# Optimization experiments

Measured on AMD Instinct MI355X. Metric: run time of the kernel, lower is better.

The kernel has to match this reference:

```python
import jax, jax.numpy as jnp
import numpy as np


def fps(xyz, npoint):
    # farthest point sampling, starts at index 0 (matches pointnet2 CUDA kernel)
    B, N, _ = xyz.shape
    def step(carry, _):
        min_d, last = carry
        last_xyz = jnp.take_along_axis(xyz, last[:, None, None], axis=1)  # [B,1,3]
        d = jnp.sum((xyz - last_xyz) ** 2, axis=-1)                        # [B,N]
        min_d = jnp.minimum(min_d, d)
        nxt = jnp.argmax(min_d, axis=1).astype(jnp.int32)
        return (min_d, nxt), last
    init = (jnp.full((B, N), 1e10, xyz.dtype), jnp.zeros((B,), jnp.int32))
    _, idx = jax.lax.scan(step, init, None, length=npoint)
    return jnp.transpose(idx)  # [B, npoint]


def ball_query(xyz, new_xyz, radius, nsample):
    # first nsample points within radius; pad with first hit (0 if none) -- CUDA semantics
    N = xyz.shape[1]
    d2 = jnp.sum((new_xyz[:, :, None, :] - xyz[:, None, :, :]) ** 2, axis=-1)  # [B,S,N]
    cand = jnp.where(d2 < radius * radius, jnp.arange(N, dtype=jnp.int32)[None, None, :], N)
    srt = jnp.sort(cand, axis=-1)[..., :nsample]
    first = srt[..., :1]
    first = jnp.where(first == N, 0, first)
    return jnp.where(srt == N, first, srt)  # [B,S,K]


def gather_nbrs(x, idx):
    # x [B,N,C], idx [B,S,K] -> [B,S,K,C]
    B, S, K = idx.shape
    flat = jnp.take_along_axis(x, idx.reshape(B, S * K, 1), axis=1)
    return flat.reshape(B, S, K, x.shape[-1])


def shared_mlp(x, layers):
    # 1x1 conv (+ folded eval-mode BN) + ReLU per layer
    for w, b in layers:
        x = jax.nn.relu(jnp.einsum('bskc,oc->bsko', x, w) + b)
    return x


def sa_module(xyz, feat, npoint, radius, nsample, layers):
    idx = fps(xyz, npoint)
    new_xyz = jnp.take_along_axis(xyz, idx[:, :, None], axis=1)  # [B,S,3]
    gidx = ball_query(xyz, new_xyz, radius, nsample)
    grouped = gather_nbrs(xyz, gidx) - new_xyz[:, :, None, :]    # centered local xyz
    if feat is not None:
        grouped = jnp.concatenate([grouped, gather_nbrs(feat, gidx)], axis=-1)
    x = shared_mlp(grouped, layers)
    return new_xyz, jnp.max(x, axis=2)  # max-pool over neighbors -> [B,S,Cout]


def sa_module_all(xyz, feat, layers):
    # GroupAll: concat raw (uncentered) xyz with features, one group of all points
    x = jnp.concatenate([xyz, feat], axis=-1)[:, None]  # [B,1,N,3+C]
    x = shared_mlp(x, layers)
    return jnp.max(x, axis=2)[:, 0]  # [B,Cout]


def _forward(data, ws):
    B, T, N, _ = data.shape
    xyz = data.reshape(B * T, N, 3)
    xyz, feat = sa_module(xyz, None, 256, 0.2, 32, ws[0])
    xyz, feat = sa_module(xyz, feat, 128, 0.4, 32, ws[1])
    out = sa_module_all(xyz, feat, ws[2])
    return out.reshape(B, T, -1)


DIMS = [(3, 64), (64, 64), (64, 128), (131, 128), (128, 128), (128, 256), (259, 256), (256, 512), (512, 1024)]
NAMES = ['1_0', '1_1', '1_2', '2_0', '2_1', '2_2', '3_0', '3_1', '3_2']


def setup_inputs() -> dict:
    key = jax.random.key(0)
    keys = jax.random.split(key, 1 + 2 * len(DIMS))
    inp = {'data': jax.random.normal(keys[0], (4, 8, 4096, 3), jnp.float32)}
    for i, ((cin, cout), nm) in enumerate(zip(DIMS, NAMES)):
        inp['w' + nm] = jax.random.normal(keys[1 + 2 * i], (cout, cin), jnp.float32) / np.sqrt(cin).astype(np.float32)
        inp['b' + nm] = jax.random.normal(keys[2 + 2 * i], (cout,), jnp.float32) * 0.02
    return inp


def reference(data, w1_0, b1_0, w1_1, b1_1, w1_2, b1_2,
              w2_0, b2_0, w2_1, b2_1, w2_2, b2_2,
              w3_0, b3_0, w3_1, b3_1, w3_2, b3_2):
    ws = [[(w1_0, b1_0), (w1_1, b1_1), (w1_2, b1_2)],
          [(w2_0, b2_0), (w2_1, b2_1), (w2_2, b2_2)],
          [(w3_0, b3_0), (w3_1, b3_1), (w3_2, b3_2)]]
    return _forward(data, ws)
```

## Files before the change

### kernel.cpp

```cpp
#include <hip/hip_runtime.h>
#include <hip/hip_bf16.h>
#include <cstdint>
#include <cstddef>

#define BT 32
#define N1 4096
#define S1 256
#define S2 128
#define KNB 32

typedef __attribute__((ext_vector_type(8))) short short8;
typedef __attribute__((ext_vector_type(4))) float f32x4;

__device__ __forceinline__ float sqdist(float ax, float ay, float az,
                                        float bx, float by, float bz) {
    float dx = __fsub_rn(ax, bx), dy = __fsub_rn(ay, by), dz = __fsub_rn(az, bz);
    return __fadd_rn(__fadd_rn(__fmul_rn(dx, dx), __fmul_rn(dy, dy)), __fmul_rn(dz, dz));
}

__device__ __forceinline__ unsigned short f2bf(float f) {
    unsigned u = __float_as_uint(f);
    return (unsigned short)((u + 0x7FFFu + ((u >> 16) & 1u)) >> 16);
}
__device__ __forceinline__ float bf2f(unsigned short h) {
    return __uint_as_float(((unsigned)h) << 16);
}

__device__ __forceinline__ unsigned long long packvi(float v, int idx) {
    return ((unsigned long long)__float_as_uint(v) << 32) | (unsigned)(~idx);
}

template <int CTRL>
__device__ __forceinline__ unsigned long long dppmax(unsigned long long v) {
    int lo = (int)(unsigned)(v & 0xFFFFFFFFull);
    int hi = (int)(unsigned)(v >> 32);
    int lo2 = __builtin_amdgcn_update_dpp(0, lo, CTRL, 0xF, 0xF, false);
    int hi2 = __builtin_amdgcn_update_dpp(0, hi, CTRL, 0xF, 0xF, false);
    unsigned long long o = ((unsigned long long)(unsigned)hi2 << 32) | (unsigned)lo2;
    return o > v ? o : v;
}
#define ROR1 0x121
#define ROR2 0x122
#define ROR4 0x124
#define ROR8 0x128

__global__ __launch_bounds__(256) void fps1_kernel(const float* __restrict__ xyz,
                                                   float* __restrict__ nxz) {
    const int b = blockIdx.x, tid = threadIdx.x;
    const int lane = tid & 63, wv = tid >> 6;
    const float* X = xyz + (size_t)b * (N1 * 3);
    __shared__ float4 s4[N1];
    __shared__ unsigned long long slots[2][16];
    __shared__ float hist[S1 * 3];
    float px[16], py[16], pz[16], md[16];
    int bidx[16];
#pragma unroll
    for (int j = 0; j < 16; ++j) {
        int i = tid + 256 * j;
        float x = X[i * 3 + 0], y = X[i * 3 + 1], z = X[i * 3 + 2];
        s4[i] = make_float4(x, y, z, 0.f);
        px[j] = x; py[j] = y; pz[j] = z;
        md[j] = 1e10f;
        bidx[j] = i;
    }
    if (tid == 0) { hist[0] = X[0]; hist[1] = X[1]; hist[2] = X[2]; }
    __syncthreads();
    float4 c0 = s4[0];
    float lx = c0.x, ly = c0.y, lz = c0.z;
    for (int t = 1; t < S1; ++t) {
        float bv = -1.0f; int bi = 0;
#pragma unroll
        for (int j = 0; j < 16; ++j) {
            float d = sqdist(px[j], py[j], pz[j], lx, ly, lz);
            float m = fminf(md[j], d);
            md[j] = m;
            if (m > bv) { bv = m; bi = bidx[j]; }
        }
        unsigned long long best = packvi(bv, bi);
        best = dppmax<ROR1>(best);
        best = dppmax<ROR2>(best);
        best = dppmax<ROR4>(best);
        best = dppmax<ROR8>(best);
        if ((lane & 15) == 0) slots[t & 1][wv * 4 + (lane >> 4)] = best;
        __syncthreads();
        unsigned long long w = slots[t & 1][lane & 15];
        w = dppmax<ROR1>(w);
        w = dppmax<ROR2>(w);
        w = dppmax<ROR4>(w);
        w = dppmax<ROR8>(w);
        int vi = (int)(~(unsigned)w);
        float4 c = s4[vi];
        lx = c.x; ly = c.y; lz = c.z;
        if (tid == 0) { hist[t * 3 + 0] = lx; hist[t * 3 + 1] = ly; hist[t * 3 + 2] = lz; }
    }
    __syncthreads();
    for (int u = tid; u < S1 * 3; u += 256) nxz[(size_t)b * S1 * 3 + u] = hist[u];
}

__global__ __launch_bounds__(64) void fps2_kernel(const float* __restrict__ xyz1,
                                                  float* __restrict__ nxz2) {
    const int b = blockIdx.x, lane = threadIdx.x;
    const float* X = xyz1 + (size_t)b * (S1 * 3);
    __shared__ float4 s4[S1];
    float px[4], py[4], pz[4], md[4];
    int bidx[4];
#pragma unroll
    for (int j = 0; j < 4; ++j) {
        int i = lane + 64 * j;
        float x = X[i * 3 + 0], y = X[i * 3 + 1], z = X[i * 3 + 2];
        s4[i] = make_float4(x, y, z, 0.f);
        px[j] = x; py[j] = y; pz[j] = z;
        md[j] = 1e10f;
        bidx[j] = i;
    }
    if (lane == 0) {
        nxz2[(size_t)b * S2 * 3 + 0] = X[0];
        nxz2[(size_t)b * S2 * 3 + 1] = X[1];
        nxz2[(size_t)b * S2 * 3 + 2] = X[2];
    }
    float4 cc = s4[0];
    float lx = cc.x, ly = cc.y, lz = cc.z;
    for (int t = 1; t < S2; ++t) {
        float bv = -1.0f; int bi = 0;
#pragma unroll
        for (int j = 0; j < 4; ++j) {
            float d = sqdist(px[j], py[j], pz[j], lx, ly, lz);
            float m = fminf(md[j], d);
            md[j] = m;
            if (m > bv) { bv = m; bi = bidx[j]; }
        }
        unsigned long long best = packvi(bv, bi);
        best = dppmax<ROR1>(best);
        best = dppmax<ROR2>(best);
        best = dppmax<ROR4>(best);
        best = dppmax<ROR8>(best);
        { unsigned long long o = __shfl_xor(best, 16); best = o > best ? o : best; }
        { unsigned long long o = __shfl_xor(best, 32); best = o > best ? o : best; }
        int vi = (int)(~(unsigned)best);
        float4 c = s4[vi];
        lx = c.x; ly = c.y; lz = c.z;
        if (lane == 0) {
            float* dst = nxz2 + ((size_t)b * S2 + t) * 3;
            dst[0] = lx; dst[1] = ly; dst[2] = lz;
        }
    }
}

__global__ __launch_bounds__(256) void ballq1_kernel(const float* __restrict__ xyz,
                                                     const float* __restrict__ nxz,
                                                     int* __restrict__ gidx) {
    const int wid = (blockIdx.x * 256 + threadIdx.x) >> 6;
    const int lane = threadIdx.x & 63;
    const int b = wid >> 8;
    const float* X = xyz + (size_t)b * (N1 * 3);
    const float* C = nxz + (size_t)wid * 3;
    const float cx = C[0], cy = C[1], cz = C[2];
    const float r2 = (float)(0.2 * 0.2);
    int* G = gidx + (size_t)wid * KNB;
    int cnt = 0, first = 0;
    bool found = false;
    for (int j0 = 0; j0 < N1 && cnt < KNB; j0 += 64) {
        int j = j0 + lane;
        float d2 = sqdist(cx, cy, cz, X[j * 3 + 0], X[j * 3 + 1], X[j * 3 + 2]);
        bool hit = d2 < r2;
        unsigned long long mask = __ballot(hit);
        if (!found && mask) { first = j0 + __builtin_ctzll(mask); found = true; }
        if (hit) {
            int pos = cnt + __popcll(mask & ((1ull << lane) - 1ull));
            if (pos < KNB) G[pos] = j;
        }
        cnt += __popcll(mask);
    }
    if (cnt < KNB) {
        int pad = found ? first : 0;
        if (lane >= cnt && lane < KNB) G[lane] = pad;
    }
}

__global__ __launch_bounds__(256) void ballq2_kernel(const float* __restrict__ xyz1,
                                                     const float* __restrict__ nxz2,
                                                     int* __restrict__ gidx) {
    const int wid = (blockIdx.x * 256 + threadIdx.x) >> 6;
    const int lane = threadIdx.x & 63;
    const int b = wid >> 7;
    const float* X = xyz1 + (size_t)b * (S1 * 3);
    const float* C = nxz2 + (size_t)wid * 3;
    const float cx = C[0], cy = C[1], cz = C[2];
    const float r2 = (float)(0.4 * 0.4);
    int* G = gidx + (size_t)wid * KNB;
    int cnt = 0, first = 0;
    bool found = false;
    for (int j0 = 0; j0 < S1 && cnt < KNB; j0 += 64) {
        int j = j0 + lane;
        float d2 = sqdist(cx, cy, cz, X[j * 3 + 0], X[j * 3 + 1], X[j * 3 + 2]);
        bool hit = d2 < r2;
        unsigned long long mask = __ballot(hit);
        if (!found && mask) { first = j0 + __builtin_ctzll(mask); found = true; }
        if (hit) {
            int pos = cnt + __popcll(mask & ((1ull << lane) - 1ull));
            if (pos < KNB) G[pos] = j;
        }
        cnt += __popcll(mask);
    }
    if (cnt < KNB) {
        int pad = found ? first : 0;
        if (lane >= cnt && lane < KNB) G[lane] = pad;
    }
}

__global__ __launch_bounds__(256) void wconv_kernel(
    const float* __restrict__ w11, const float* __restrict__ w12,
    const float* __restrict__ w20, const float* __restrict__ w21,
    const float* __restrict__ w22, const float* __restrict__ w30,
    const float* __restrict__ w31, const float* __restrict__ w32,
    unsigned short* __restrict__ wb) {
    int u = blockIdx.x * 256 + threadIdx.x;
    if (u >= 823296) return;
    const float* src; int base, Kp, Ko; int perm = 0;
    if      (u < 4096)   { src = w11; base = 0;      Kp = 64;  Ko = 64;  }
    else if (u < 12288)  { src = w12; base = 4096;   Kp = 64;  Ko = 64;  }
    else if (u < 36864)  { src = w20; base = 12288;  Kp = 192; Ko = 131; perm = 128; }
    else if (u < 53248)  { src = w21; base = 36864;  Kp = 128; Ko = 128; }
    else if (u < 86016)  { src = w22; base = 53248;  Kp = 128; Ko = 128; }
    else if (u < 167936) { src = w30; base = 86016;  Kp = 320; Ko = 259; perm = 256; }
    else if (u < 299008) { src = w31; base = 167936; Kp = 256; Ko = 256; }
    else                 { src = w32; base = 299008; Kp = 512; Ko = 512; }
    int local = u - base;
    int n = local / Kp, k = local - n * Kp;
    float v;
    if (perm) {
        int ksrc = (k < perm) ? (k + 3) : ((k < perm + 3) ? (k - perm) : -1);
        v = (ksrc >= 0) ? src[(size_t)n * Ko + ksrc] : 0.f;
    } else {
        v = (k < Ko) ? src[(size_t)n * Ko + k] : 0.f;
    }
    wb[u] = f2bf(v);
}

__global__ __launch_bounds__(256) void m1_kernel(
    const float* __restrict__ xyz, const float* __restrict__ nxz,
    const int* __restrict__ g1,
    const float* __restrict__ w10, const float* __restrict__ b10,
    const unsigned short* __restrict__ w11b, const float* __restrict__ b11,
    const unsigned short* __restrict__ w12b, const float* __restrict__ b12,
    unsigned short* __restrict__ f1) {
    constexpr int AP = 72;
    __shared__ __align__(16) unsigned short As[128 * AP];
    __shared__ __align__(16) unsigned short Hs[128 * AP];
    __shared__ __align__(16) unsigned short Bs[192 * AP];
    __shared__ float sxyz[128 * 3];
    const int t = threadIdx.x;
    const int lane = t & 63, w = t >> 6;
    const int r16 = lane & 15, q = lane >> 4;
    const int m0 = blockIdx.x * 128;

    if (t < 128) {
        int row = m0 + t, bs = row >> 5, b = bs >> 8, j = g1[row];
        const float* P = xyz + ((size_t)b * N1 + j) * 3;
        const float* Cc = nxz + (size_t)bs * 3;
        sxyz[t * 3 + 0] = P[0] - Cc[0];
        sxyz[t * 3 + 1] = P[1] - Cc[1];
        sxyz[t * 3 + 2] = P[2] - Cc[2];
    }
    for (int c = t; c < 192 * 8; c += 256) {
        int row = c >> 3, ch = c & 7;
        const unsigned short* src = (row < 64) ? &w11b[row * 64 + ch * 8]
                                               : &w12b[(row - 64) * 64 + ch * 8];
        *(short8*)&Bs[row * AP + ch * 8] = *(const short8*)src;
    }
    __syncthreads();
    {
        const int r = t >> 1, half = (t & 1) * 32;
        const float x = sxyz[r * 3 + 0], y = sxyz[r * 3 + 1], z = sxyz[r * 3 + 2];
        unsigned short tmp[32];
#pragma unroll
        for (int o = 0; o < 32; ++o) {
            int oo = half + o;
            float acc = b10[oo];
            acc = fmaf(x, w10[oo * 3 + 0], acc);
            acc = fmaf(y, w10[oo * 3 + 1], acc);
            acc = fmaf(z, w10[oo * 3 + 2], acc);
            tmp[o] = f2bf(fmaxf(acc, 0.f));
        }
#pragma unroll
        for (int c2 = 0; c2 < 4; ++c2)
            *(short8*)&As[r * AP + half + c2 * 8] = *(short8*)&tmp[c2 * 8];
    }
    __syncthreads();
    {
        f32x4 acc[2][4];
#pragma unroll
        for (int i = 0; i < 2; ++i)
#pragma unroll
            for (int j = 0; j < 4; ++j) acc[i][j] = (f32x4){0.f, 0.f, 0.f, 0.f};
#pragma unroll
        for (int kk = 0; kk < 64; kk += 32) {
            short8 a0 = *(const short8*)&As[(w * 32 + r16) * AP + kk + q * 8];
            short8 a1 = *(const short8*)&As[(w * 32 + 16 + r16) * AP + kk + q * 8];
#pragma unroll
            for (int j = 0; j < 4; ++j) {
                short8 bf = *(const short8*)&Bs[(j * 16 + r16) * AP + kk + q * 8];
                acc[0][j] = __builtin_amdgcn_mfma_f32_16x16x32_bf16(a0, bf, acc[0][j], 0, 0, 0);
                acc[1][j] = __builtin_amdgcn_mfma_f32_16x16x32_bf16(a1, bf, acc[1][j], 0, 0, 0);
            }
        }
#pragma unroll
        for (int i = 0; i < 2; ++i)
#pragma unroll
            for (int j = 0; j < 4; ++j) {
                int col = j * 16 + r16;
                float bv = b11[col];
#pragma unroll
                for (int r = 0; r < 4; ++r) {
                    int row = w * 32 + i * 16 + q * 4 + r;
                    Hs[row * AP + col] = f2bf(fmaxf(acc[i][j][r] + bv, 0.f));
                }
            }
    }
    __syncthreads();
    {
        f32x4 acc[2][8];
#pragma unroll
        for (int i = 0; i < 2; ++i)
#pragma unroll
            for (int j = 0; j < 8; ++j) acc[i][j] = (f32x4){0.f, 0.f, 0.f, 0.f};
#pragma unroll
        for (int kk = 0; kk < 64; kk += 32) {
            short8 a0 = *(const short8*)&Hs[(w * 32 + r16) * AP + kk + q * 8];
            short8 a1 = *(const short8*)&Hs[(w * 32 + 16 + r16) * AP + kk + q * 8];
#pragma unroll
            for (int j = 0; j < 8; ++j) {
                short8 bf = *(const short8*)&Bs[(64 + j * 16 + r16) * AP + kk + q * 8];
                acc[0][j] = __builtin_amdgcn_mfma_f32_16x16x32_bf16(a0, bf, acc[0][j], 0, 0, 0);
                acc[1][j] = __builtin_amdgcn_mfma_f32_16x16x32_bf16(a1, bf, acc[1][j], 0, 0, 0);
            }
        }
#pragma unroll
        for (int j = 0; j < 8; ++j) {
            int col = j * 16 + r16;
            float bv = b12[col];
            float mv = 0.f;
#pragma unroll
            for (int i = 0; i < 2; ++i)
#pragma unroll
                for (int r = 0; r < 4; ++r)
                    mv = fmaxf(mv, acc[i][j][r] + bv);
            mv = fmaxf(mv, __shfl_xor(mv, 16));
            mv = fmaxf(mv, __shfl_xor(mv, 32));
            if (q == 0)
                f1[(size_t)((m0 >> 5) + w) * 128 + col] = f2bf(mv);
        }
    }
}

__global__ __launch_bounds__(256) void m2_kernel(
    const float* __restrict__ xyz1, const float* __restrict__ nxz2,
    const int* __restrict__ g2, const unsigned short* __restrict__ f1,
    const unsigned short* __restrict__ w20p, const float* __restrict__ b20,
    const unsigned short* __restrict__ w21b, const float* __restrict__ b21,
    const unsigned short* __restrict__ w22b, const float* __restrict__ b22,
    unsigned short* __restrict__ f2) {
    constexpr int AP = 72, HP = 136;
    __shared__ __align__(16) unsigned short smem[36864];
    unsigned short* R1 = smem;
    unsigned short* R2 = smem + 18432;
    unsigned short* As = R1;
    unsigned short* Bs = R1 + 9216;
    unsigned short* W21 = R1;
    unsigned short* H1 = R2;
    unsigned short* H2 = R1;
    unsigned short* Bs2 = R2;
    __shared__ int ribase[128];
    __shared__ unsigned short sxb[128 * 3];
    const int t = threadIdx.x;
    const int lane = t & 63, w = t >> 6;
    const int r16 = lane & 15, q = lane >> 4;
    const int m0 = blockIdx.x * 128;

    if (t < 128) {
        int row = m0 + t, bs = row >> 5, b = bs >> 7, j = g2[row];
        ribase[t] = (b * 256 + j) * 128;
        const float* P = xyz1 + ((size_t)b * S1 + j) * 3;
        const float* Cc = nxz2 + (size_t)bs * 3;
        sxb[t * 3 + 0] = f2bf(P[0] - Cc[0]);
// ... 352 lines not shown
    const float* w21 = (const float*)d_in[9];  const float* b21 = (const float*)d_in[10];
    const float* w22 = (const float*)d_in[11]; const float* b22 = (const float*)d_in[12];
    const float* w30 = (const float*)d_in[13]; const float* b30 = (const float*)d_in[14];
    const float* w31 = (const float*)d_in[15]; const float* b31 = (const float*)d_in[16];
    const float* w32 = (const float*)d_in[17]; const float* b32 = (const float*)d_in[18];
    float* out = (float*)d_out;

    char* ws = (char*)d_ws;
    size_t off = 0;
    auto alloc = [&](size_t bytes) -> void* {
        void* p = ws + off;
        off += (bytes + 255) & ~(size_t)255;
        return p;
    };
    float* nxz1 = (float*)alloc((size_t)BT * S1 * 3 * 4);
    int*   g1   = (int*)  alloc((size_t)BT * S1 * KNB * 4);
    float* nxz2 = (float*)alloc((size_t)BT * S2 * 3 * 4);
    int*   g2   = (int*)  alloc((size_t)BT * S2 * KNB * 4);
    unsigned short* wb  = (unsigned short*)alloc((size_t)823296 * 2);
    unsigned short* f1  = (unsigned short*)alloc((size_t)8192 * 128 * 2);
    unsigned short* f2  = (unsigned short*)alloc((size_t)4096 * 256 * 2);
    unsigned short* C1  = (unsigned short*)alloc((size_t)4096 * 256 * 2);
    unsigned short* C2  = (unsigned short*)alloc((size_t)4096 * 512 * 2);

    const unsigned short* w11b = wb + 0;
    const unsigned short* w12b = wb + 4096;
    const unsigned short* w20p = wb + 12288;
    const unsigned short* w21b = wb + 36864;
    const unsigned short* w22b = wb + 53248;
    const unsigned short* w30p = wb + 86016;
    const unsigned short* w31b = wb + 167936;
    const unsigned short* w32b = wb + 299008;

    wconv_kernel<<<(823296 + 255) / 256, 256, 0, stream>>>(w11, w12, w20, w21, w22, w30, w31, w32, wb);

    fps1_kernel<<<BT, 256, 0, stream>>>(data, nxz1);
    ballq1_kernel<<<(BT * S1) / 4, 256, 0, stream>>>(data, nxz1, g1);
    m1_kernel<<<262144 / 128, 256, 0, stream>>>(data, nxz1, g1, w10, b10, w11b, b11, w12b, b12, f1);
    fps2_kernel<<<BT, 64, 0, stream>>>(nxz1, nxz2);
    ballq2_kernel<<<(BT * S2) / 4, 256, 0, stream>>>(nxz1, nxz2, g2);
    m2_kernel<<<131072 / 128, 256, 0, stream>>>(nxz1, nxz2, g2, f1, w20p, b20, w21b, b21, w22b, b22, f2);
    l30_kernel<<<dim3(4096 / 128, 2), 256, 0, stream>>>(nxz2, f2, w30p, b30, C1);
    mfma_gemm<64><<<dim3(4096 / 64, 4), 256, 0, stream>>>(C1, w31b, b31, C2, 4096, 512, 256);
    gemm_pool128<<<dim3(4096 / 128, 8), 256, 0, stream>>>(C2, w32b, b32, out);
}
```

Measured before the change: 487.8 us.

## Merge independent stages into shared launches to overlap FPS with other work

Independent stages now share launches through a block-index split. FPS1 runs alongside the weight conversion, FPS2 alongside ball query 1, and ball query 2 alongside the first MLP stage. The aim is to hide the long serial FPS kernels behind parallel work and to cut launch count and idle GPU time between dependent launches. Risks: the merged kernels share a register and LDS footprint, so the large FPS1 shared array may limit occupancy of the wconv blocks, and the slow FPS blocks may still dominate the critical path.

```diff
diff --git a/kernel.cpp b/kernel.cpp
--- a/kernel.cpp
+++ b/kernel.cpp
@@ -44,206 +44,205 @@
 #define ROR4 0x124
 #define ROR8 0x128
 
-__global__ __launch_bounds__(256) void fps1_kernel(const float* __restrict__ xyz,
-                                                   float* __restrict__ nxz) {
-    const int b = blockIdx.x, tid = threadIdx.x;
-    const int lane = tid & 63, wv = tid >> 6;
-    const float* X = xyz + (size_t)b * (N1 * 3);
-    __shared__ float4 s4[N1];
-    __shared__ unsigned long long slots[2][16];
-    __shared__ float hist[S1 * 3];
-    float px[16], py[16], pz[16], md[16];
-    int bidx[16];
-#pragma unroll
-    for (int j = 0; j < 16; ++j) {
-        int i = tid + 256 * j;
-        float x = X[i * 3 + 0], y = X[i * 3 + 1], z = X[i * 3 + 2];
-        s4[i] = make_float4(x, y, z, 0.f);
-        px[j] = x; py[j] = y; pz[j] = z;
-        md[j] = 1e10f;
-        bidx[j] = i;
-    }
-    if (tid == 0) { hist[0] = X[0]; hist[1] = X[1]; hist[2] = X[2]; }
-    __syncthreads();
-    float4 c0 = s4[0];
-    float lx = c0.x, ly = c0.y, lz = c0.z;
-    for (int t = 1; t < S1; ++t) {
-        float bv = -1.0f; int bi = 0;
-#pragma unroll
-        for (int j = 0; j < 16; ++j) {
-            float d = sqdist(px[j], py[j], pz[j], lx, ly, lz);
-            float m = fminf(md[j], d);
-            md[j] = m;
-            if (m > bv) { bv = m; bi = bidx[j]; }
-        }
-        unsigned long long best = packvi(bv, bi);
-        best = dppmax<ROR1>(best);
-        best = dppmax<ROR2>(best);
-        best = dppmax<ROR4>(best);
-        best = dppmax<ROR8>(best);
-        if ((lane & 15) == 0) slots[t & 1][wv * 4 + (lane >> 4)] = best;
-        __syncthreads();
-        unsigned long long w = slots[t & 1][lane & 15];
-        w = dppmax<ROR1>(w);
-        w = dppmax<ROR2>(w);
-        w = dppmax<ROR4>(w);
-        w = dppmax<ROR8>(w);
-        int vi = (int)(~(unsigned)w);
-        float4 c = s4[vi];
-        lx = c.x; ly = c.y; lz = c.z;
-        if (tid == 0) { hist[t * 3 + 0] = lx; hist[t * 3 + 1] = ly; hist[t * 3 + 2] = lz; }
-    }
-    __syncthreads();
-    for (int u = tid; u < S1 * 3; u += 256) nxz[(size_t)b * S1 * 3 + u] = hist[u];
-}
-
-__global__ __launch_bounds__(64) void fps2_kernel(const float* __restrict__ xyz1,
-                                                  float* __restrict__ nxz2) {
-    const int b = blockIdx.x, lane = threadIdx.x;
-    const float* X = xyz1 + (size_t)b * (S1 * 3);
-    __shared__ float4 s4[S1];
-    float px[4], py[4], pz[4], md[4];
-    int bidx[4];
-#pragma unroll
-    for (int j = 0; j < 4; ++j) {
-        int i = lane + 64 * j;
-        float x = X[i * 3 + 0], y = X[i * 3 + 1], z = X[i * 3 + 2];
-        s4[i] = make_float4(x, y, z, 0.f);
-        px[j] = x; py[j] = y; pz[j] = z;
-        md[j] = 1e10f;
-        bidx[j] = i;
-    }
-    if (lane == 0) {
-        nxz2[(size_t)b * S2 * 3 + 0] = X[0];
-        nxz2[(size_t)b * S2 * 3 + 1] = X[1];
-        nxz2[(size_t)b * S2 * 3 + 2] = X[2];
-    }
-    float4 cc = s4[0];
-    float lx = cc.x, ly = cc.y, lz = cc.z;
-    for (int t = 1; t < S2; ++t) {
-        float bv = -1.0f; int bi = 0;
-#pragma unroll
-        for (int j = 0; j < 4; ++j) {
-            float d = sqdist(px[j], py[j], pz[j], lx, ly, lz);
-            float m = fminf(md[j], d);
-            md[j] = m;
-            if (m > bv) { bv = m; bi = bidx[j]; }
-        }
-        unsigned long long best = packvi(bv, bi);
-        best = dppmax<ROR1>(best);
-        best = dppmax<ROR2>(best);
-        best = dppmax<ROR4>(best);
-        best = dppmax<ROR8>(best);
-        { unsigned long long o = __shfl_xor(best, 16); best = o > best ? o : best; }
-        { unsigned long long o = __shfl_xor(best, 32); best = o > best ? o : best; }
-        int vi = (int)(~(unsigned)best);
-        float4 c = s4[vi];
-        lx = c.x; ly = c.y; lz = c.z;
-        if (lane == 0) {
-            float* dst = nxz2 + ((size_t)b * S2 + t) * 3;
-            dst[0] = lx; dst[1] = ly; dst[2] = lz;
-        }
-    }
-}
-
-__global__ __launch_bounds__(256) void ballq1_kernel(const float* __restrict__ xyz,
-                                                     const float* __restrict__ nxz,
-                                                     int* __restrict__ gidx) {
-    const int wid = (blockIdx.x * 256 + threadIdx.x) >> 6;
-    const int lane = threadIdx.x & 63;
-    const int b = wid >> 8;
-    const float* X = xyz + (size_t)b * (N1 * 3);
-    const float* C = nxz + (size_t)wid * 3;
-    const float cx = C[0], cy = C[1], cz = C[2];
-    const float r2 = (float)(0.2 * 0.2);
-    int* G = gidx + (size_t)wid * KNB;
-    int cnt = 0, first = 0;
-    bool found = false;
-    for (int j0 = 0; j0 < N1 && cnt < KNB; j0 += 64) {
-        int j = j0 + lane;
-        float d2 = sqdist(cx, cy, cz, X[j * 3 + 0], X[j * 3 + 1], X[j * 3 + 2]);
-        bool hit = d2 < r2;
-        unsigned long long mask = __ballot(hit);
-        if (!found && mask) { first = j0 + __builtin_ctzll(mask); found = true; }
-        if (hit) {
-            int pos = cnt + __popcll(mask & ((1ull << lane) - 1ull));
-            if (pos < KNB) G[pos] = j;
-        }
-        cnt += __popcll(mask);
-    }
-    if (cnt < KNB) {
-        int pad = found ? first : 0;
-        if (lane >= cnt && lane < KNB) G[lane] = pad;
-    }
-}
-
-__global__ __launch_bounds__(256) void ballq2_kernel(const float* __restrict__ xyz1,
-                                                     const float* __restrict__ nxz2,
-                                                     int* __restrict__ gidx) {
-    const int wid = (blockIdx.x * 256 + threadIdx.x) >> 6;
-    const int lane = threadIdx.x & 63;
-    const int b = wid >> 7;
-    const float* X = xyz1 + (size_t)b * (S1 * 3);
-    const float* C = nxz2 + (size_t)wid * 3;
-    const float cx = C[0], cy = C[1], cz = C[2];
-    const float r2 = (float)(0.4 * 0.4);
-    int* G = gidx + (size_t)wid * KNB;
-    int cnt = 0, first = 0;
-    bool found = false;
-    for (int j0 = 0; j0 < S1 && cnt < KNB; j0 += 64) {
-        int j = j0 + lane;
-        float d2 = sqdist(cx, cy, cz, X[j * 3 + 0], X[j * 3 + 1], X[j * 3 + 2]);
-        bool hit = d2 < r2;
-        unsigned long long mask = __ballot(hit);
-        if (!found && mask) { first = j0 + __builtin_ctzll(mask); found = true; }
-        if (hit) {
-            int pos = cnt + __popcll(mask & ((1ull << lane) - 1ull));
-            if (pos < KNB) G[pos] = j;
-        }
-        cnt += __popcll(mask);
-    }
-    if (cnt < KNB) {
-        int pad = found ? first : 0;
-        if (lane >= cnt && lane < KNB) G[lane] = pad;
-    }
-}
-
-__global__ __launch_bounds__(256) void wconv_kernel(
+__global__ __launch_bounds__(256) void fps1_wconv_kernel(
+    const float* __restrict__ xyz, float* __restrict__ nxz,
     const float* __restrict__ w11, const float* __restrict__ w12,
     const float* __restrict__ w20, const float* __restrict__ w21,
     const float* __restrict__ w22, const float* __restrict__ w30,
     const float* __restrict__ w31, const float* __restrict__ w32,
     unsigned short* __restrict__ wb) {
-    int u = blockIdx.x * 256 + threadIdx.x;
-    if (u >= 823296) return;
-    const float* src; int base, Kp, Ko; int perm = 0;
-    if      (u < 4096)   { src = w11; base = 0;      Kp = 64;  Ko = 64;  }
-    else if (u < 12288)  { src = w12; base = 4096;   Kp = 64;  Ko = 64;  }
-    else if (u < 36864)  { src = w20; base = 12288;  Kp = 192; Ko = 131; perm = 128; }
-    else if (u < 53248)  { src = w21; base = 36864;  Kp = 128; Ko = 128; }
-    else if (u < 86016)  { src = w22; base = 53248;  Kp = 128; Ko = 128; }
-    else if (u < 167936) { src = w30; base = 86016;  Kp = 320; Ko = 259; perm = 256; }
-    else if (u < 299008) { src = w31; base = 167936; Kp = 256; Ko = 256; }
-    else                 { src = w32; base = 299008; Kp = 512; Ko = 512; }
-    int local = u - base;
-    int n = local / Kp, k = local - n * Kp;
-    float v;
-    if (perm) {
-        int ksrc = (k < perm) ? (k + 3) : ((k < perm + 3) ? (k - perm) : -1);
-        v = (ksrc >= 0) ? src[(size_t)n * Ko + ksrc] : 0.f;
+    if (blockIdx.x < 32) {
+        const int b = blockIdx.x, tid = threadIdx.x;
+        const int lane = tid & 63, wv = tid >> 6;
+        const float* X = xyz + (size_t)b * (N1 * 3);
+        __shared__ float4 s4[N1];
+        __shared__ unsigned long long slots[2][16];
+        __shared__ float hist[S1 * 3];
+        float px[16], py[16], pz[16], md[16];
+        int bidx[16];
+#pragma unroll
+        for (int j = 0; j < 16; ++j) {
+            int i = tid + 256 * j;
+            float x = X[i * 3 + 0], y = X[i * 3 + 1], z = X[i * 3 + 2];
+            s4[i] = make_float4(x, y, z, 0.f);
+            px[j] = x; py[j] = y; pz[j] = z;
+            md[j] = 1e10f;
+            bidx[j] = i;
+        }
+        if (tid == 0) { hist[0] = X[0]; hist[1] = X[1]; hist[2] = X[2]; }
+        __syncthreads();
+        float4 c0 = s4[0];
+        float lx = c0.x, ly = c0.y, lz = c0.z;
+        for (int t = 1; t < S1; ++t) {
+            float bv = -1.0f; int bi = 0;
+#pragma unroll
+            for (int j = 0; j < 16; ++j) {
+                float d = sqdist(px[j], py[j], pz[j], lx, ly, lz);
+                float m = fminf(md[j], d);
+                md[j] = m;
+                if (m > bv) { bv = m; bi = bidx[j]; }
+            }
+            unsigned long long best = packvi(bv, bi);
+            best = dppmax<ROR1>(best);
+            best = dppmax<ROR2>(best);
+            best = dppmax<ROR4>(best);
+            best = dppmax<ROR8>(best);
+            if ((lane & 15) == 0) slots[t & 1][wv * 4 + (lane >> 4)] = best;
+            __syncthreads();
+            unsigned long long w = slots[t & 1][lane & 15];
+            w = dppmax<ROR1>(w);
+            w = dppmax<ROR2>(w);
+            w = dppmax<ROR4>(w);
+            w = dppmax<ROR8>(w);
+            int vi = (int)(~(unsigned)w);
+            float4 c = s4[vi];
+            lx = c.x; ly = c.y; lz = c.z;
+            if (tid == 0) { hist[t * 3 + 0] = lx; hist[t * 3 + 1] = ly; hist[t * 3 + 2] = lz; }
+        }
+        __syncthreads();
+        for (int u = tid; u < S1 * 3; u += 256) nxz[(size_t)b * S1 * 3 + u] = hist[u];
     } else {
-        v = (k < Ko) ? src[(size_t)n * Ko + k] : 0.f;
-    }
-    wb[u] = f2bf(v);
-}
-
-__global__ __launch_bounds__(256) void m1_kernel(
+        int u = (blockIdx.x - 32) * 256 + threadIdx.x;
+        if (u >= 823296) return;
+        const float* src; int base, Kp, Ko; int perm = 0;
+        if      (u < 4096)   { src = w11; base = 0;      Kp = 64;  Ko = 64;  }
+        else if (u < 12288)  { src = w12; base = 4096;   Kp = 64;  Ko = 64;  }
+        else if (u < 36864)  { src = w20; base = 12288;  Kp = 192; Ko = 131; perm = 128; }
+        else if (u < 53248)  { src = w21; base = 36864;  Kp = 128; Ko = 128; }
+        else if (u < 86016)  { src = w22; base = 53248;  Kp = 128; Ko = 128; }
+        else if (u < 167936) { src = w30; base = 86016;  Kp = 320; Ko = 259; perm = 256; }
+        else if (u < 299008) { src = w31; base = 167936; Kp = 256; Ko = 256; }
+        else                 { src = w32; base = 299008; Kp = 512; Ko = 512; }
+        int local = u - base;
+        int n = local / Kp, k = local - n * Kp;
+        float v;
+        if (perm) {
+            int ksrc = (k < perm) ? (k + 3) : ((k < perm + 3) ? (k - perm) : -1);
+            v = (ksrc >= 0) ? src[(size_t)n * Ko + ksrc] : 0.f;
+        } else {
+            v = (k < Ko) ? src[(size_t)n * Ko + k] : 0.f;
+        }
+        wb[u] = f2bf(v);
+    }
+}
+
+__global__ __launch_bounds__(256) void ballq1_fps2_kernel(
+    const float* __restrict__ xyz, const float* __restrict__ nxz,
+    int* __restrict__ gidx, float* __restrict__ nxz2) {
+    if (blockIdx.x < 32) {
+        if (threadIdx.x >= 64) return;
+        const int b = blockIdx.x, lane = threadIdx.x;
+        const float* X = nxz + (size_t)b * (S1 * 3);
+        __shared__ float4 s4[S1];
+        float px[4], py[4], pz[4], md[4];
+        int bidx[4];
+#pragma unroll
+        for (int j = 0; j < 4; ++j) {
+            int i = lane + 64 * j;
+            float x = X[i * 3 + 0], y = X[i * 3 + 1], z = X[i * 3 + 2];
+            s4[i] = make_float4(x, y, z, 0.f);
+            px[j] = x; py[j] = y; pz[j] = z;
+            md[j] = 1e10f;
+            bidx[j] = i;
+        }
+        if (lane == 0) {
+            nxz2[(size_t)b * S2 * 3 + 0] = X[0];
+            nxz2[(size_t)b * S2 * 3 + 1] = X[1];
+            nxz2[(size_t)b * S2 * 3 + 2] = X[2];
+        }
+        float4 cc = s4[0];
+        float lx = cc.x, ly = cc.y, lz = cc.z;
+        for (int t = 1; t < S2; ++t) {
+            float bv = -1.0f; int bi = 0;
+#pragma unroll
+            for (int j = 0; j < 4; ++j) {
+                float d = sqdist(px[j], py[j], pz[j], lx, ly, lz);
+                float m = fminf(md[j], d);
+                md[j] = m;
+                if (m > bv) { bv = m; bi = bidx[j]; }
+            }
+            unsigned long long best = packvi(bv, bi);
+            best = dppmax<ROR1>(best);
+            best = dppmax<ROR2>(best);
+            best = dppmax<ROR4>(best);
+            best = dppmax<ROR8>(best);
+            { unsigned long long o = __shfl_xor(best, 16); best = o > best ? o : best; }
+            { unsigned long long o = __shfl_xor(best, 32); best = o > best ? o : best; }
+            int vi = (int)(~(unsigned)best);
+            float4 c = s4[vi];
+            lx = c.x; ly = c.y; lz = c.z;
+            if (lane == 0) {
+                float* dst = nxz2 + ((size_t)b * S2 + t) * 3;
+                dst[0] = lx; dst[1] = ly; dst[2] = lz;
+            }
+        }
+    } else {
+        const int wid = ((blockIdx.x - 32) * 256 + threadIdx.x) >> 6;
+        const int lane = threadIdx.x & 63;
+        const int b = wid >> 8;
+        const float* X = xyz + (size_t)b * (N1 * 3);
+        const float* C = nxz + (size_t)wid * 3;
+        const float cx = C[0], cy = C[1], cz = C[2];
+        const float r2 = (float)(0.2 * 0.2);
+        int* G = gidx + (size_t)wid * KNB;
+        int cnt = 0, first = 0;
+        bool found = false;
+        for (int j0 = 0; j0 < N1 && cnt < KNB; j0 += 64) {
+            int j = j0 + lane;
+            float d2 = sqdist(cx, cy, cz, X[j * 3 + 0], X[j * 3 + 1], X[j * 3 + 2]);
+            bool hit = d2 < r2;
+            unsigned long long mask = __ballot(hit);
+            if (!found && mask) { first = j0 + __builtin_ctzll(mask); found = true; }
+            if (hit) {
+                int pos = cnt + __popcll(mask & ((1ull << lane) - 1ull));
+                if (pos < KNB) G[pos] = j;
+            }
+            cnt += __popcll(mask);
+        }
+        if (cnt < KNB) {
+            int pad = found ? first : 0;
+            if (lane >= cnt && lane < KNB) G[lane] = pad;
+        }
+    }
+}
+
+__global__ __launch_bounds__(256) void m1_bq2_kernel(
     const float* __restrict__ xyz, const float* __restrict__ nxz,
     const int* __restrict__ g1,
     const float* __restrict__ w10, const float* __restrict__ b10,
     const unsigned short* __restrict__ w11b, const float* __restrict__ b11,
     const unsigned short* __restrict__ w12b, const float* __restrict__ b12,
-    unsigned short* __restrict__ f1) {
+    unsigned short* __restrict__ f1,
+    const float* __restrict__ nxz2, int* __restrict__ g2) {
+    if (blockIdx.x >= 2048) {
+        const int wid = ((blockIdx.x - 2048) * 256 + threadIdx.x) >> 6;
+        const int lane = threadIdx.x & 63;
+        const int b = wid >> 7;
+        const float* X = nxz + (size_t)b * (S1 * 3);
+        const float* C = nxz2 + (size_t)wid * 3;
+        const float cx = C[0], cy = C[1], cz = C[2];
+        const float r2 = (float)(0.4 * 0.4);
+        int* G = g2 + (size_t)wid * KNB;
+        int cnt = 0, first = 0;
+        bool found = false;
+        for (int j0 = 0; j0 < S1 && cnt < KNB; j0 += 64) {
+            int j = j0 + lane;
+            float d2 = sqdist(cx, cy, cz, X[j * 3 + 0], X[j * 3 + 1], X[j * 3 + 2]);
+            bool hit = d2 < r2;
+            unsigned long long mask = __ballot(hit);
+            if (!found && mask) { first = j0 + __builtin_ctzll(mask); found = true; }
+            if (hit) {
+                int pos = cnt + __popcll(mask & ((1ull << lane) - 1ull));
+                if (pos < KNB) G[pos] = j;
+            }
+            cnt += __popcll(mask);
+        }
+        if (cnt < KNB) {
+            int pad = found ? first : 0;
+            if (lane >= cnt && lane < KNB) G[lane] = pad;
+        }
+        return;
+    }
     constexpr int AP = 72;
     __shared__ __align__(16) unsigned short As[128 * AP];
     __shared__ __align__(16) unsigned short Hs[128 * AP];
@@ -768,13 +767,11 @@
     const unsigned short* w31b = wb + 167936;
     const unsigned short* w32b = wb + 299008;
 
-    wconv_kernel<<<(823296 + 255) / 256, 256, 0, stream>>>(w11, w12, w20, w21, w22, w30, w31, w32, wb);
-
-    fps1_kernel<<<BT, 256, 0, stream>>>(data, nxz1);
-    ballq1_kernel<<<(BT * S1) / 4, 256, 0, stream>>>(data, nxz1, g1);
-    m1_kernel<<<262144 / 128, 256, 0, stream>>>(data, nxz1, g1, w10, b10, w11b, b11, w12b, b12, f1);
-    fps2_kernel<<<BT, 64, 0, stream>>>(nxz1, nxz2);
-    ballq2_kernel<<<(BT * S2) / 4, 256, 0, stream>>>(nxz1, nxz2, g2);
+    fps1_wconv_kernel<<<32 + 3216, 256, 0, stream>>>(
+        data, nxz1, w11, w12, w20, w21, w22, w30, w31, w32, wb);
+    ballq1_fps2_kernel<<<32 + 2048, 256, 0, stream>>>(data, nxz1, g1, nxz2);
+    m1_bq2_kernel<<<2048 + 1024, 256, 0, stream>>>(
+        data, nxz1, g1, w10, b10, w11b, b11, w12b, b12, f1, nxz2, g2);
     m2_kernel<<<131072 / 128, 256, 0, stream>>>(nxz1, nxz2, g2, f1, w20p, b20, w21b, b21, w22b, b22, f2);
     l30_kernel<<<dim3(4096 / 128, 2), 256, 0, stream>>>(nxz2, f2, w30p, b30, C1);
     mfma_gemm<64><<<dim3(4096 / 64, 4), 256, 0, stream>>>(C1, w31b, b31, C2, 4096, 512, 256);
```

Result: faster. 450.7 us (-7.6%).

## Co-schedule FPS with weight conversion and MLP1 via block-range kernel merging

Applied to the files above, without the earlier changes.

Merges the weight-conversion kernel into the first FPS kernel, and the second FPS kernel into the first-stage MLP kernel. Each merged kernel picks its role from the block index, so the latency-bound 32-block FPS work runs alongside independent bulk work instead of serially, which also removes two launches. The cost is a larger combined shared-memory footprint per block, which can lower occupancy for the MLP blocks, and FPS blocks may be scheduled behind or among the other blocks.

```diff
diff --git a/kernel.cpp b/kernel.cpp
--- a/kernel.cpp
+++ b/kernel.cpp
@@ -44,105 +44,85 @@
 #define ROR4 0x124
 #define ROR8 0x128
 
-__global__ __launch_bounds__(256) void fps1_kernel(const float* __restrict__ xyz,
-                                                   float* __restrict__ nxz) {
-    const int b = blockIdx.x, tid = threadIdx.x;
-    const int lane = tid & 63, wv = tid >> 6;
-    const float* X = xyz + (size_t)b * (N1 * 3);
-    __shared__ float4 s4[N1];
-    __shared__ unsigned long long slots[2][16];
-    __shared__ float hist[S1 * 3];
-    float px[16], py[16], pz[16], md[16];
-    int bidx[16];
-#pragma unroll
-    for (int j = 0; j < 16; ++j) {
-        int i = tid + 256 * j;
-        float x = X[i * 3 + 0], y = X[i * 3 + 1], z = X[i * 3 + 2];
-        s4[i] = make_float4(x, y, z, 0.f);
-        px[j] = x; py[j] = y; pz[j] = z;
-        md[j] = 1e10f;
-        bidx[j] = i;
-    }
-    if (tid == 0) { hist[0] = X[0]; hist[1] = X[1]; hist[2] = X[2]; }
-    __syncthreads();
-    float4 c0 = s4[0];
-    float lx = c0.x, ly = c0.y, lz = c0.z;
-    for (int t = 1; t < S1; ++t) {
-        float bv = -1.0f; int bi = 0;
+__global__ __launch_bounds__(256) void fps1_wconv_kernel(
+    const float* __restrict__ xyz, float* __restrict__ nxz,
+    const float* __restrict__ w11, const float* __restrict__ w12,
+    const float* __restrict__ w20, const float* __restrict__ w21,
+    const float* __restrict__ w22, const float* __restrict__ w30,
+    const float* __restrict__ w31, const float* __restrict__ w32,
+    unsigned short* __restrict__ wb) {
+    if (blockIdx.x < 32) {
+        const int b = blockIdx.x, tid = threadIdx.x;
+        const int lane = tid & 63, wv = tid >> 6;
+        const float* X = xyz + (size_t)b * (N1 * 3);
+        __shared__ float4 s4[N1];
+        __shared__ unsigned long long slots[2][16];
+        __shared__ float hist[S1 * 3];
+        float px[16], py[16], pz[16], md[16];
+        int bidx[16];
 #pragma unroll
         for (int j = 0; j < 16; ++j) {
-            float d = sqdist(px[j], py[j], pz[j], lx, ly, lz);
-            float m = fminf(md[j], d);
-            md[j] = m;
-            if (m > bv) { bv = m; bi = bidx[j]; }
-        }
-        unsigned long long best = packvi(bv, bi);
-        best = dppmax<ROR1>(best);
-        best = dppmax<ROR2>(best);
-        best = dppmax<ROR4>(best);
-        best = dppmax<ROR8>(best);
-        if ((lane & 15) == 0) slots[t & 1][wv * 4 + (lane >> 4)] = best;
-        __syncthreads();
-        unsigned long long w = slots[t & 1][lane & 15];
-        w = dppmax<ROR1>(w);
-        w = dppmax<ROR2>(w);
-        w = dppmax<ROR4>(w);
-        w = dppmax<ROR8>(w);
-        int vi = (int)(~(unsigned)w);
-        float4 c = s4[vi];
-        lx = c.x; ly = c.y; lz = c.z;
-        if (tid == 0) { hist[t * 3 + 0] = lx; hist[t * 3 + 1] = ly; hist[t * 3 + 2] = lz; }
-    }
-    __syncthreads();
-    for (int u = tid; u < S1 * 3; u += 256) nxz[(size_t)b * S1 * 3 + u] = hist[u];
-}
-
-__global__ __launch_bounds__(64) void fps2_kernel(const float* __restrict__ xyz1,
-                                                  float* __restrict__ nxz2) {
-    const int b = blockIdx.x, lane = threadIdx.x;
-    const float* X = xyz1 + (size_t)b * (S1 * 3);
-    __shared__ float4 s4[S1];
-    float px[4], py[4], pz[4], md[4];
-    int bidx[4];
-#pragma unroll
-    for (int j = 0; j < 4; ++j) {
-        int i = lane + 64 * j;
-        float x = X[i * 3 + 0], y = X[i * 3 + 1], z = X[i * 3 + 2];
-        s4[i] = make_float4(x, y, z, 0.f);
-        px[j] = x; py[j] = y; pz[j] = z;
-        md[j] = 1e10f;
-        bidx[j] = i;
-    }
-    if (lane == 0) {
-        nxz2[(size_t)b * S2 * 3 + 0] = X[0];
-        nxz2[(size_t)b * S2 * 3 + 1] = X[1];
-        nxz2[(size_t)b * S2 * 3 + 2] = X[2];
-    }
-    float4 cc = s4[0];
-    float lx = cc.x, ly = cc.y, lz = cc.z;
-    for (int t = 1; t < S2; ++t) {
-        float bv = -1.0f; int bi = 0;
-#pragma unroll
-        for (int j = 0; j < 4; ++j) {
-            float d = sqdist(px[j], py[j], pz[j], lx, ly, lz);
-            float m = fminf(md[j], d);
-            md[j] = m;
-            if (m > bv) { bv = m; bi = bidx[j]; }
-        }
-        unsigned long long best = packvi(bv, bi);
-        best = dppmax<ROR1>(best);
-        best = dppmax<ROR2>(best);
-        best = dppmax<ROR4>(best);
-        best = dppmax<ROR8>(best);
-        { unsigned long long o = __shfl_xor(best, 16); best = o > best ? o : best; }
-        { unsigned long long o = __shfl_xor(best, 32); best = o > best ? o : best; }
-        int vi = (int)(~(unsigned)best);
-        float4 c = s4[vi];
-        lx = c.x; ly = c.y; lz = c.z;
-        if (lane == 0) {
-            float* dst = nxz2 + ((size_t)b * S2 + t) * 3;
-            dst[0] = lx; dst[1] = ly; dst[2] = lz;
-        }
+            int i = tid + 256 * j;
+            float x = X[i * 3 + 0], y = X[i * 3 + 1], z = X[i * 3 + 2];
+            s4[i] = make_float4(x, y, z, 0.f);
+            px[j] = x; py[j] = y; pz[j] = z;
+            md[j] = 1e10f;
+            bidx[j] = i;
+        }
+        if (tid == 0) { hist[0] = X[0]; hist[1] = X[1]; hist[2] = X[2]; }
+        __syncthreads();
+        float4 c0 = s4[0];
+        float lx = c0.x, ly = c0.y, lz = c0.z;
+        for (int t = 1; t < S1; ++t) {
+            float bv = -1.0f; int bi = 0;
+#pragma unroll
+            for (int j = 0; j < 16; ++j) {
+                float d = sqdist(px[j], py[j], pz[j], lx, ly, lz);
+                float m = fminf(md[j], d);
+                md[j] = m;
+                if (m > bv) { bv = m; bi = bidx[j]; }
+            }
+            unsigned long long best = packvi(bv, bi);
+            best = dppmax<ROR1>(best);
+            best = dppmax<ROR2>(best);
+            best = dppmax<ROR4>(best);
+            best = dppmax<ROR8>(best);
+            if ((lane & 15) == 0) slots[t & 1][wv * 4 + (lane >> 4)] = best;
+            __syncthreads();
+            unsigned long long w = slots[t & 1][lane & 15];
+            w = dppmax<ROR1>(w);
+            w = dppmax<ROR2>(w);
+            w = dppmax<ROR4>(w);
+            w = dppmax<ROR8>(w);
+            int vi = (int)(~(unsigned)w);
+            float4 c = s4[vi];
+            lx = c.x; ly = c.y; lz = c.z;
+            if (tid == 0) { hist[t * 3 + 0] = lx; hist[t * 3 + 1] = ly; hist[t * 3 + 2] = lz; }
+        }
+        __syncthreads();
+        for (int u = tid; u < S1 * 3; u += 256) nxz[(size_t)b * S1 * 3 + u] = hist[u];
+    } else {
+        int u = (blockIdx.x - 32) * 256 + threadIdx.x;
+        if (u >= 823296) return;
+        const float* src; int base, Kp, Ko; int perm = 0;
+        if      (u < 4096)   { src = w11; base = 0;      Kp = 64;  Ko = 64;  }
+        else if (u < 12288)  { src = w12; base = 4096;   Kp = 64;  Ko = 64;  }
+        else if (u < 36864)  { src = w20; base = 12288;  Kp = 192; Ko = 131; perm = 128; }
+        else if (u < 53248)  { src = w21; base = 36864;  Kp = 128; Ko = 128; }
+        else if (u < 86016)  { src = w22; base = 53248;  Kp = 128; Ko = 128; }
+        else if (u < 167936) { src = w30; base = 86016;  Kp = 320; Ko = 259; perm = 256; }
+        else if (u < 299008) { src = w31; base = 167936; Kp = 256; Ko = 256; }
+        else                 { src = w32; base = 299008; Kp = 512; Ko = 512; }
+        int local = u - base;
+        int n = local / Kp, k = local - n * Kp;
+        float v;
+        if (perm) {
+            int ksrc = (k < perm) ? (k + 3) : ((k < perm + 3) ? (k - perm) : -1);
+            v = (ksrc >= 0) ? src[(size_t)n * Ko + ksrc] : 0.f;
+        } else {
+            v = (k < Ko) ? src[(size_t)n * Ko + k] : 0.f;
+        }
+        wb[u] = f2bf(v);
     }
 }
 
@@ -177,6 +157,172 @@
     }
 }
 
+__global__ __launch_bounds__(256) void m1_fps2_kernel(
+    const float* __restrict__ xyz, const float* __restrict__ nxz,
+    const int* __restrict__ g1,
+    const float* __restrict__ w10, const float* __restrict__ b10,
+    const unsigned short* __restrict__ w11b, const float* __restrict__ b11,
+    const unsigned short* __restrict__ w12b, const float* __restrict__ b12,
+    unsigned short* __restrict__ f1,
+    float* __restrict__ nxz2) {
+    if (blockIdx.x < 32) {
+        if (threadIdx.x >= 64) return;
+        const int b = blockIdx.x, lane = threadIdx.x;
+        const float* X = nxz + (size_t)b * (S1 * 3);
+        __shared__ float4 s4f[S1];
+        float px[4], py[4], pz[4], md[4];
+        int bidx[4];
+#pragma unroll
+        for (int j = 0; j < 4; ++j) {
+            int i = lane + 64 * j;
+            float x = X[i * 3 + 0], y = X[i * 3 + 1], z = X[i * 3 + 2];
+            s4f[i] = make_float4(x, y, z, 0.f);
+            px[j] = x; py[j] = y; pz[j] = z;
+            md[j] = 1e10f;
+            bidx[j] = i;
+        }
+        if (lane == 0) {
+            nxz2[(size_t)b * S2 * 3 + 0] = X[0];
+            nxz2[(size_t)b * S2 * 3 + 1] = X[1];
+            nxz2[(size_t)b * S2 * 3 + 2] = X[2];
+        }
+        float4 cc = s4f[0];
+        float lx = cc.x, ly = cc.y, lz = cc.z;
+        for (int t = 1; t < S2; ++t) {
+            float bv = -1.0f; int bi = 0;
+#pragma unroll
+            for (int j = 0; j < 4; ++j) {
+                float d = sqdist(px[j], py[j], pz[j], lx, ly, lz);
+                float m = fminf(md[j], d);
+                md[j] = m;
+                if (m > bv) { bv = m; bi = bidx[j]; }
+            }
+            unsigned long long best = packvi(bv, bi);
+            best = dppmax<ROR1>(best);
+            best = dppmax<ROR2>(best);
+            best = dppmax<ROR4>(best);
+            best = dppmax<ROR8>(best);
+            { unsigned long long o = __shfl_xor(best, 16); best = o > best ? o : best; }
+            { unsigned long long o = __shfl_xor(best, 32); best = o > best ? o : best; }
+            int vi = (int)(~(unsigned)best);
+            float4 c = s4f[vi];
+            lx = c.x; ly = c.y; lz = c.z;
+            if (lane == 0) {
+                float* dst = nxz2 + ((size_t)b * S2 + t) * 3;
+                dst[0] = lx; dst[1] = ly; dst[2] = lz;
+            }
+        }
+        return;
+    }
+    constexpr int AP = 72;
+    __shared__ __align__(16) unsigned short As[128 * AP];
+    __shared__ __align__(16) unsigned short Hs[128 * AP];
+    __shared__ __align__(16) unsigned short Bs[192 * AP];
+    __shared__ float sxyz[128 * 3];
+    const int t = threadIdx.x;
+    const int lane = t & 63, w = t >> 6;
+    const int r16 = lane & 15, q = lane >> 4;
+    const int m0 = (blockIdx.x - 32) * 128;
+
+    if (t < 128) {
+        int row = m0 + t, bs = row >> 5, b = bs >> 8, j = g1[row];
+        const float* P = xyz + ((size_t)b * N1 + j) * 3;
+        const float* Cc = nxz + (size_t)bs * 3;
+        sxyz[t * 3 + 0] = P[0] - Cc[0];
+        sxyz[t * 3 + 1] = P[1] - Cc[1];
+        sxyz[t * 3 + 2] = P[2] - Cc[2];
+    }
+    for (int c = t; c < 192 * 8; c += 256) {
+        int row = c >> 3, ch = c & 7;
+        const unsigned short* src = (row < 64) ? &w11b[row * 64 + ch * 8]
+                                               : &w12b[(row - 64) * 64 + ch * 8];
+        *(short8*)&Bs[row * AP + ch * 8] = *(const short8*)src;
+    }
+    __syncthreads();
+    {
+        const int r = t >> 1, half = (t & 1) * 32;
+        const float x = sxyz[r * 3 + 0], y = sxyz[r * 3 + 1], z = sxyz[r * 3 + 2];
+        unsigned short tmp[32];
+#pragma unroll
+        for (int o = 0; o < 32; ++o) {
+            int oo = half + o;
+            float acc = b10[oo];
+            acc = fmaf(x, w10[oo * 3 + 0], acc);
+            acc = fmaf(y, w10[oo * 3 + 1], acc);
+            acc = fmaf(z, w10[oo * 3 + 2], acc);
+            tmp[o] = f2bf(fmaxf(acc, 0.f));
+        }
+#pragma unroll
+        for (int c2 = 0; c2 < 4; ++c2)
+            *(short8*)&As[r * AP + half + c2 * 8] = *(short8*)&tmp[c2 * 8];
+    }
+    __syncthreads();
+    {
+        f32x4 acc[2][4];
+#pragma unroll
+        for (int i = 0; i < 2; ++i)
+#pragma unroll
+            for (int j = 0; j < 4; ++j) acc[i][j] = (f32x4){0.f, 0.f, 0.f, 0.f};
+#pragma unroll
+        for (int kk = 0; kk < 64; kk += 32) {
+            short8 a0 = *(const short8*)&As[(w * 32 + r16) * AP + kk + q * 8];
+            short8 a1 = *(const short8*)&As[(w * 32 + 16 + r16) * AP + kk + q * 8];
+#pragma unroll
+            for (int j = 0; j < 4; ++j) {
+                short8 bf = *(const short8*)&Bs[(j * 16 + r16) * AP + kk + q * 8];
+                acc[0][j] = __builtin_amdgcn_mfma_f32_16x16x32_bf16(a0, bf, acc[0][j], 0, 0, 0);
+                acc[1][j] = __builtin_amdgcn_mfma_f32_16x16x32_bf16(a1, bf, acc[1][j], 0, 0, 0);
+            }
+        }
+#pragma unroll
+        for (int i = 0; i < 2; ++i)
+#pragma unroll
+            for (int j = 0; j < 4; ++j) {
+                int col = j * 16 + r16;
+                float bv = b11[col];
+#pragma unroll
+                for (int r = 0; r < 4; ++r) {
+                    int row = w * 32 + i * 16 + q * 4 + r;
+                    Hs[row * AP + col] = f2bf(fmaxf(acc[i][j][r] + bv, 0.f));
+                }
+            }
+    }
+    __syncthreads();
+    {
+        f32x4 acc[2][8];
+#pragma unroll
+        for (int i = 0; i < 2; ++i)
+#pragma unroll
+            for (int j = 0; j < 8; ++j) acc[i][j] = (f32x4){0.f, 0.f, 0.f, 0.f};
+#pragma unroll
+        for (int kk = 0; kk < 64; kk += 32) {
+            short8 a0 = *(const short8*)&Hs[(w * 32 + r16) * AP + kk + q * 8];
+            short8 a1 = *(const short8*)&Hs[(w * 32 + 16 + r16) * AP + kk + q * 8];
+#pragma unroll
+            for (int j = 0; j < 8; ++j) {
+                short8 bf = *(const short8*)&Bs[(64 + j * 16 + r16) * AP + kk + q * 8];
+                acc[0][j] = __builtin_amdgcn_mfma_f32_16x16x32_bf16(a0, bf, acc[0][j], 0, 0, 0);
+                acc[1][j] = __builtin_amdgcn_mfma_f32_16x16x32_bf16(a1, bf, acc[1][j], 0, 0, 0);
+            }
+        }
+#pragma unroll
+        for (int j = 0; j < 8; ++j) {
+            int col = j * 16 + r16;
+            float bv = b12[col];
+            float mv = 0.f;
+#pragma unroll
+            for (int i = 0; i < 2; ++i)
+#pragma unroll
+                for (int r = 0; r < 4; ++r)
+                    mv = fmaxf(mv, acc[i][j][r] + bv);
+            mv = fmaxf(mv, __shfl_xor(mv, 16));
+            mv = fmaxf(mv, __shfl_xor(mv, 32));
+            if (q == 0)
+                f1[(size_t)((m0 >> 5) + w) * 128 + col] = f2bf(mv);
+        }
+    }
+}
+
 __global__ __launch_bounds__(256) void ballq2_kernel(const float* __restrict__ xyz1,
                                                      const float* __restrict__ nxz2,
                                                      int* __restrict__ gidx) {
@@ -205,151 +351,6 @@
     if (cnt < KNB) {
         int pad = found ? first : 0;
         if (lane >= cnt && lane < KNB) G[lane] = pad;
-    }
-}
-
-__global__ __launch_bounds__(256) void wconv_kernel(
-    const float* __restrict__ w11, const float* __restrict__ w12,
-    const float* __restrict__ w20, const float* __restrict__ w21,
-    const float* __restrict__ w22, const float* __restrict__ w30,
-    const float* __restrict__ w31, const float* __restrict__ w32,
-    unsigned short* __restrict__ wb) {
-    int u = blockIdx.x * 256 + threadIdx.x;
-    if (u >= 823296) return;
-    const float* src; int base, Kp, Ko; int perm = 0;
-    if      (u < 4096)   { src = w11; base = 0;      Kp = 64;  Ko = 64;  }
-    else if (u < 12288)  { src = w12; base = 4096;   Kp = 64;  Ko = 64;  }
-    else if (u < 36864)  { src = w20; base = 12288;  Kp = 192; Ko = 131; perm = 128; }
-    else if (u < 53248)  { src = w21; base = 36864;  Kp = 128; Ko = 128; }
-    else if (u < 86016)  { src = w22; base = 53248;  Kp = 128; Ko = 128; }
-    else if (u < 167936) { src = w30; base = 86016;  Kp = 320; Ko = 259; perm = 256; }
-    else if (u < 299008) { src = w31; base = 167936; Kp = 256; Ko = 256; }
-    else                 { src = w32; base = 299008; Kp = 512; Ko = 512; }
-    int local = u - base;
-    int n = local / Kp, k = local - n * Kp;
-    float v;
-    if (perm) {
-        int ksrc = (k < perm) ? (k + 3) : ((k < perm + 3) ? (k - perm) : -1);
-        v = (ksrc >= 0) ? src[(size_t)n * Ko + ksrc] : 0.f;
-    } else {
-        v = (k < Ko) ? src[(size_t)n * Ko + k] : 0.f;
-    }
-    wb[u] = f2bf(v);
-}
-
-__global__ __launch_bounds__(256) void m1_kernel(
-    const float* __restrict__ xyz, const float* __restrict__ nxz,
-    const int* __restrict__ g1,
-    const float* __restrict__ w10, const float* __restrict__ b10,
-    const unsigned short* __restrict__ w11b, const float* __restrict__ b11,
-    const unsigned short* __restrict__ w12b, const float* __restrict__ b12,
-    unsigned short* __restrict__ f1) {
-    constexpr int AP = 72;
-    __shared__ __align__(16) unsigned short As[128 * AP];
-    __shared__ __align__(16) unsigned short Hs[128 * AP];
-    __shared__ __align__(16) unsigned short Bs[192 * AP];
-    __shared__ float sxyz[128 * 3];
-    const int t = threadIdx.x;
-    const int lane = t & 63, w = t >> 6;
-    const int r16 = lane & 15, q = lane >> 4;
-    const int m0 = blockIdx.x * 128;
-
-    if (t < 128) {
-        int row = m0 + t, bs = row >> 5, b = bs >> 8, j = g1[row];
-        const float* P = xyz + ((size_t)b * N1 + j) * 3;
-        const float* Cc = nxz + (size_t)bs * 3;
-        sxyz[t * 3 + 0] = P[0] - Cc[0];
-        sxyz[t * 3 + 1] = P[1] - Cc[1];
-        sxyz[t * 3 + 2] = P[2] - Cc[2];
-    }
-    for (int c = t; c < 192 * 8; c += 256) {
-        int row = c >> 3, ch = c & 7;
-        const unsigned short* src = (row < 64) ? &w11b[row * 64 + ch * 8]
-                                               : &w12b[(row - 64) * 64 + ch * 8];
-        *(short8*)&Bs[row * AP + ch * 8] = *(const short8*)src;
-    }
-    __syncthreads();
-    {
-        const int r = t >> 1, half = (t & 1) * 32;
-        const float x = sxyz[r * 3 + 0], y = sxyz[r * 3 + 1], z = sxyz[r * 3 + 2];
-        unsigned short tmp[32];
-#pragma unroll
-        for (int o = 0; o < 32; ++o) {
-            int oo = half + o;
-            float acc = b10[oo];
-            acc = fmaf(x, w10[oo * 3 + 0], acc);
-            acc = fmaf(y, w10[oo * 3 + 1], acc);
-            acc = fmaf(z, w10[oo * 3 + 2], acc);
-            tmp[o] = f2bf(fmaxf(acc, 0.f));
-        }
-#pragma unroll
-        for (int c2 = 0; c2 < 4; ++c2)
-            *(short8*)&As[r * AP + half + c2 * 8] = *(short8*)&tmp[c2 * 8];
-    }
-    __syncthreads();
-    {
-        f32x4 acc[2][4];
-#pragma unroll
-        for (int i = 0; i < 2; ++i)
-#pragma unroll
-            for (int j = 0; j < 4; ++j) acc[i][j] = (f32x4){0.f, 0.f, 0.f, 0.f};
-#pragma unroll
-        for (int kk = 0; kk < 64; kk += 32) {
-            short8 a0 = *(const short8*)&As[(w * 32 + r16) * AP + kk + q * 8];
-            short8 a1 = *(const short8*)&As[(w * 32 + 16 + r16) * AP + kk + q * 8];
-#pragma unroll
-            for (int j = 0; j < 4; ++j) {
-                short8 bf = *(const short8*)&Bs[(j * 16 + r16) * AP + kk + q * 8];
-                acc[0][j] = __builtin_amdgcn_mfma_f32_16x16x32_bf16(a0, bf, acc[0][j], 0, 0, 0);
-                acc[1][j] = __builtin_amdgcn_mfma_f32_16x16x32_bf16(a1, bf, acc[1][j], 0, 0, 0);
-            }
-        }
-#pragma unroll
-        for (int i = 0; i < 2; ++i)
-#pragma unroll
-            for (int j = 0; j < 4; ++j) {
-                int col = j * 16 + r16;
-                float bv = b11[col];
-#pragma unroll
-                for (int r = 0; r < 4; ++r) {
-                    int row = w * 32 + i * 16 + q * 4 + r;
-                    Hs[row * AP + col] = f2bf(fmaxf(acc[i][j][r] + bv, 0.f));
-                }
-            }
-    }
-    __syncthreads();
-    {
-        f32x4 acc[2][8];
-#pragma unroll
-        for (int i = 0; i < 2; ++i)
-#pragma unroll
-            for (int j = 0; j < 8; ++j) acc[i][j] = (f32x4){0.f, 0.f, 0.f, 0.f};
-#pragma unroll
-        for (int kk = 0; kk < 64; kk += 32) {
-            short8 a0 = *(const short8*)&Hs[(w * 32 + r16) * AP + kk + q * 8];
-            short8 a1 = *(const short8*)&Hs[(w * 32 + 16 + r16) * AP + kk + q * 8];
-#pragma unroll
-            for (int j = 0; j < 8; ++j) {
-                short8 bf = *(const short8*)&Bs[(64 + j * 16 + r16) * AP + kk + q * 8];
-                acc[0][j] = __builtin_amdgcn_mfma_f32_16x16x32_bf16(a0, bf, acc[0][j], 0, 0, 0);
-                acc[1][j] = __builtin_amdgcn_mfma_f32_16x16x32_bf16(a1, bf, acc[1][j], 0, 0, 0);
-            }
-        }
-#pragma unroll
-        for (int j = 0; j < 8; ++j) {
-            int col = j * 16 + r16;
-            float bv = b12[col];
-            float mv = 0.f;
-#pragma unroll
-            for (int i = 0; i < 2; ++i)
-#pragma unroll
-                for (int r = 0; r < 4; ++r)
-                    mv = fmaxf(mv, acc[i][j][r] + bv);
-            mv = fmaxf(mv, __shfl_xor(mv, 16));
-            mv = fmaxf(mv, __shfl_xor(mv, 32));
-            if (q == 0)
-                f1[(size_t)((m0 >> 5) + w) * 128 + col] = f2bf(mv);
-        }
     }
 }
 
@@ -768,12 +769,11 @@
     const unsigned short* w31b = wb + 167936;
     const unsigned short* w32b = wb + 299008;
 
-    wconv_kernel<<<(823296 + 255) / 256, 256, 0, stream>>>(w11, w12, w20, w21, w22, w30, w31, w32, wb);
-
-    fps1_kernel<<<BT, 256, 0, stream>>>(data, nxz1);
+    fps1_wconv_kernel<<<32 + 3216, 256, 0, stream>>>(
+        data, nxz1, w11, w12, w20, w21, w22, w30, w31, w32, wb);
     ballq1_kernel<<<(BT * S1) / 4, 256, 0, stream>>>(data, nxz1, g1);
-    m1_kernel<<<262144 / 128, 256, 0, stream>>>(data, nxz1, g1, w10, b10, w11b, b11, w12b, b12, f1);
-    fps2_kernel<<<BT, 64, 0, stream>>>(nxz1, nxz2);
+    m1_fps2_kernel<<<32 + 2048, 256, 0, stream>>>(
+        data, nxz1, g1, w10, b10, w11b, b11, w12b, b12, f1, nxz2);
     ballq2_kernel<<<(BT * S2) / 4, 256, 0, stream>>>(nxz1, nxz2, g2);
     m2_kernel<<<131072 / 128, 256, 0, stream>>>(nxz1, nxz2, g2, f1, w20p, b20, w21b, b21, w22b, b22, f2);
     l30_kernel<<<dim3(4096 / 128, 2), 256, 0, stream>>>(nxz2, f2, w30p, b30, C1);
```

After: 449.9 us. -7.8%, faster.
